# Kernel tuning notes

Measured on AMD Instinct MI355X. Metric: run time of the kernel, lower is better.

Reference implementation:

```python
import jax, jax.numpy as jnp
import numpy as np
import math

K = 3          # kernel_size
P_GEM = 3.0    # GeM power
EPS_GEM = 1e-6
EPS_NORM = 1e-12


def _l2n(x, axis):
    n = jnp.sqrt(jnp.sum(x * x, axis=axis, keepdims=True))
    return x / jnp.maximum(n, EPS_NORM)


def setup_inputs() -> dict:
    key = jax.random.key(0)
    ks = jax.random.split(key, 7)
    b, hw, c, nc = 32, 196, 768, 4096
    hidden = c  # mlp_ratio = 1
    return {
        "patch_tokens": jax.random.normal(ks[0], (b, hw, c), dtype=jnp.float32),
        "fc1_w": jax.random.normal(ks[1], (c, hidden), dtype=jnp.float32) * 0.02,
        "fc1_b": jnp.zeros((hidden,), dtype=jnp.float32),
        "fc2_w": jax.random.normal(ks[2], (hidden, c), dtype=jnp.float32) * 0.02,
        "fc2_b": jnp.zeros((c,), dtype=jnp.float32),
        "head_w": jax.random.normal(ks[3], (c, nc), dtype=jnp.float32) * 0.02,
        "head_b": jnp.zeros((nc,), dtype=jnp.float32),
    }


def reference(patch_tokens, fc1_w, fc1_b, fc2_w, fc2_b, head_w, head_b):
    b, hw, c = patch_tokens.shape
    h = w = int(math.sqrt(hw))

    # ---- SpaceSelfAware: pad -> unfold (3x3 local windows) -> multiply ----
    img = jnp.transpose(patch_tokens, (0, 2, 1)).reshape(b, c, h, w)
    # ZeroPad2d((left=1, right=1, top=2, bottom=0)) for kernel_size=3
    padded = jnp.pad(img, ((0, 0), (0, 0), (K - 1, 0), (K // 2, K // 2)))
    # stack the 9 shifted views, row-major over (ki, kj) matching nn.Unfold
    wins = jnp.stack(
        [padded[:, :, ki:ki + h, kj:kj + w] for ki in range(K) for kj in range(K)],
        axis=2,
    )  # (b, c, 9, h, w)
    y = wins.reshape(b, c, K, K, hw)
    y = jnp.transpose(y, (0, 4, 1, 2, 3))  # (b, hw, c, K, K)
    ssa = patch_tokens[:, :, :, None, None] * y  # (b, hw, c, K, K)

    # ---- space_fusion: L2Norm(dim=1) then GeM(p=3) over the KxK window ----
    ssa = _l2n(ssa, axis=1)
    pooled = jnp.mean(jnp.clip(ssa, EPS_GEM, None) ** P_GEM, axis=(-2, -1)) ** (1.0 / P_GEM)  # (b, hw, c)

    # ---- residual + L2 normalize over channels + Mlp ----
    tokens = pooled + patch_tokens
    tokens = _l2n(tokens, axis=-1)
    hdn = jax.nn.gelu(tokens @ fc1_w + fc1_b, approximate=False)
    tokens = hdn @ fc2_w + fc2_b  # (b, hw, c)

    # ---- GeMHead: GeM(p=3) over tokens, linear to nc, L2 normalize ----
    g = jnp.mean(jnp.clip(tokens, EPS_GEM, None) ** P_GEM, axis=1) ** (1.0 / P_GEM)  # (b, c)
    desc = g @ head_w + head_b  # (b, nc)
    desc = _l2n(desc, axis=-1)
    return desc
```

## Files before the change

kernel.cpp:

```cpp
#include <hip/hip_runtime.h>
#include <hip/hip_bf16.h>
#include <math.h>

#define B   32
#define P   196
#define C   768
#define NC  4096
#define HH  14
#define KSPLIT 24
#define NT  12
#define M6  6272
#define TW  (768 * 32)
#define TM  (M6 * 32)

typedef _Float16 half8 __attribute__((ext_vector_type(8)));
typedef _Float16 half4 __attribute__((ext_vector_type(4)));
typedef float f32x4 __attribute__((ext_vector_type(4)));

#define GLOAD_LDS16(g, l)                                                      \
    __builtin_amdgcn_global_load_lds(                                          \
        (const __attribute__((address_space(1))) void*)(g),                    \
        (__attribute__((address_space(3))) void*)(l), 16, 0, 0)

__global__ __launch_bounds__(256) void k_ssa(const float* __restrict__ t,
                                             float* __restrict__ pre) {
    const int b = blockIdx.y, c0 = blockIdx.x * 16;
    __shared__ float xp_[256 * 16];
    __shared__ float part[4][9][16];
    __shared__ float inv_norm[9][16];
    const int tid = threadIdx.x;
    const int cc = tid & 15, g = tid >> 4, wv = tid >> 6;

#pragma unroll
    for (int q = 0; q < 16; ++q) xp_[q * 256 + tid] = 0.0f;
    __syncthreads();

    for (int idx = tid; idx < 784; idx += 256) {
        const int p = idx >> 2, c = (idx & 3) * 4;
        const int i = p / HH, j = p % HH;
        *(float4*)&xp_[((i + 2) * 16 + (j + 1)) * 16 + c] =
            *(const float4*)&t[((size_t)b * P + p) * C + c0 + c];
    }
    __syncthreads();

    float s[9] = {};
    {
        int i = 0, j = g;
        if (j >= HH) { j -= HH; i = 1; }
        for (int p = g; p < P; p += 16) {
            const int base = ((i + 2) * 16 + (j + 1)) * 16 + cc;
            const float xp = xp_[base];
            const float xp2 = xp * xp;
#pragma unroll
            for (int k = 0; k < 9; ++k) {
                const int off = ((k / 3) - 2) * 16 + (k % 3) - 1;
                const float nb = xp_[base + off * 16];
                s[k] += xp2 * nb * nb;
            }
            j += 2; ++i;
            if (j >= HH) { j -= HH; ++i; }
        }
    }
#pragma unroll
    for (int k = 0; k < 9; ++k) {
        float r = s[k];
        r += __shfl_xor(r, 16);
        r += __shfl_xor(r, 32);
        s[k] = r;
    }
    if ((tid & 63) < 16) {
#pragma unroll
        for (int k = 0; k < 9; ++k) part[wv][k][cc] = s[k];
    }
    __syncthreads();
    if (tid < 144) {
        const int k = tid >> 4, c2 = tid & 15;
        const float t4 = part[0][k][c2] + part[1][k][c2] +
                         part[2][k][c2] + part[3][k][c2];
        inv_norm[k][c2] = 1.0f / fmaxf(sqrtf(t4), 1e-12f);
    }
    __syncthreads();

    float invn[9];
#pragma unroll
    for (int k = 0; k < 9; ++k) invn[k] = inv_norm[k][cc];

    {
        int i = 0, j = g;
        if (j >= HH) { j -= HH; i = 1; }
        for (int p = g; p < P; p += 16) {
            const int base = ((i + 2) * 16 + (j + 1)) * 16 + cc;
            const float xp = xp_[base];
            float acc = 0.0f;
#pragma unroll
            for (int k = 0; k < 9; ++k) {
                const int off = ((k / 3) - 2) * 16 + (k % 3) - 1;
                const float v = xp * xp_[base + off * 16];
                const float u = fmaxf(v * invn[k], 1e-6f);
                acc += u * u * u;
            }
            pre[((size_t)b * P + p) * C + c0 + cc] =
                cbrtf(acc * (1.0f / 9.0f)) + xp;
            j += 2; ++i;
            if (j >= HH) { j -= HH; ++i; }
        }
    }
}

__global__ __launch_bounds__(256) void k_rownorm(const float* __restrict__ in,
                                                 _Float16* __restrict__ outP) {
    const int row = blockIdx.x;
    const float* r = in + (size_t)row * C;
    const int tid = threadIdx.x;
    float vals[3];
    float s = 0.0f;
#pragma unroll
    for (int q = 0; q < 3; ++q) {
        vals[q] = r[tid + q * 256];
        s += vals[q] * vals[q];
    }
    __shared__ float partial[4];
    __shared__ float inv;
    __shared__ _Float16 nrm[C];
#pragma unroll
    for (int off = 32; off > 0; off >>= 1) s += __shfl_xor(s, off);
    if ((tid & 63) == 0) partial[tid >> 6] = s;
    __syncthreads();
    if (tid == 0)
        inv = 1.0f / fmaxf(sqrtf(partial[0] + partial[1] + partial[2] + partial[3]), 1e-12f);
    __syncthreads();
#pragma unroll
    for (int q = 0; q < 3; ++q)
        nrm[tid + q * 256] = (_Float16)(vals[q] * inv);
    __syncthreads();
    if (tid < 96) {
        const half8 v = *(const half8*)&nrm[tid * 8];
        const int kb = tid >> 2;
        *(half8*)&outP[(size_t)kb * TM + (size_t)row * 32 + (tid & 3) * 8] = v;
    }
}

__global__ __launch_bounds__(256) void k_wt(const float* __restrict__ W,
                                            _Float16* __restrict__ WtP) {
    __shared__ float tt[32][33];
    const int k0 = blockIdx.x * 32, n0 = blockIdx.y * 32;
    const int r = threadIdx.x / 32, c = threadIdx.x % 32;
#pragma unroll
    for (int q = 0; q < 4; ++q)
        tt[r + q * 8][c] = W[(size_t)(k0 + r + q * 8) * C + n0 + c];
    __syncthreads();
    const int nl = threadIdx.x >> 3, h = threadIdx.x & 7;
    const int n = n0 + nl;
    half4 v;
#pragma unroll
    for (int j = 0; j < 4; ++j) v[j] = (_Float16)tt[h * 4 + j][nl];
    *(half4*)&WtP[(size_t)blockIdx.x * TW + (size_t)n * 32 + h * 4] = v;
}

template <bool GELU>
__global__ __launch_bounds__(256) void k_mfma_gemm(
    const _Float16* __restrict__ TokP,
    const _Float16* __restrict__ WtP,
    const float* __restrict__ bias,
    void* __restrict__ Cout) {
    __shared__ _Float16 lA[3][2][64][32];
    __shared__ _Float16 lB[3][2][64][32];
    const int tid = threadIdx.x;
    const int w = tid >> 6, l = tid & 63;
    const int l15 = l & 15, lk = l >> 4;

    const int lid = blockIdx.x;
    int vm, vn;
    if (lid < 1152) { vm = (lid / 96) * 8 + (lid & 7); vn = (lid % 96) >> 3; }
    else            { const int r = lid - 1152; vm = 96 + r / 12; vn = r % 12; }
    const int m0 = vm * 64, n0 = vn * 64;
    const int wn = (w & 1) * 32, wm = (w >> 1) * 32;

    f32x4 acc[2][2] = {};

    const int kbsel = w & 1;
    const bool isB = (w >= 2);
    const _Float16* srcBase =
        isB ? (TokP + (size_t)m0 * 32) : (WtP + (size_t)n0 * 32);
    const size_t tileStride = isB ? (size_t)TM : (size_t)TW;
    _Float16* dst0 = isB ? &lB[0][kbsel][0][0] : &lA[0][kbsel][0][0];

#define ISSUE(tt, bf_)                                                         \
    {   const _Float16* s_ = srcBase + (size_t)(2 * (tt) + kbsel) * tileStride;\
        _Float16* d_ = dst0 + (size_t)(bf_) * 4096;                            \
        GLOAD_LDS16(s_ + l * 8,        d_ + l * 8);                            \
        GLOAD_LDS16(s_ + 512 + l * 8,  d_ + 512 + l * 8);                      \
        GLOAD_LDS16(s_ + 1024 + l * 8, d_ + 1024 + l * 8);                     \
        GLOAD_LDS16(s_ + 1536 + l * 8, d_ + 1536 + l * 8); }

    ISSUE(0, 0); ISSUE(1, 1); ISSUE(2, 2);

    for (int t = 0; t < NT; ++t) {
        if (t < NT - 2)       asm volatile("s_waitcnt vmcnt(8)" ::: "memory");
        else if (t == NT - 2) asm volatile("s_waitcnt vmcnt(4)" ::: "memory");
        else                  asm volatile("s_waitcnt vmcnt(0)" ::: "memory");
        __builtin_amdgcn_s_barrier();
        __builtin_amdgcn_sched_barrier(0);

        const int buf = t % 3;
#pragma unroll
        for (int kk = 0; kk < 2; ++kk) {
            half8 af[2], bf[2];
#pragma unroll
            for (int fa = 0; fa < 2; ++fa)
                af[fa] = *(const half8*)&lA[buf][kk][wn + fa * 16 + l15][lk * 8];
#pragma unroll
            for (int fb = 0; fb < 2; ++fb)
                bf[fb] = *(const half8*)&lB[buf][kk][wm + fb * 16 + l15][lk * 8];
#pragma unroll
            for (int fa = 0; fa < 2; ++fa)
#pragma unroll
                for (int fb = 0; fb < 2; ++fb)
                    acc[fa][fb] = __builtin_amdgcn_mfma_f32_16x16x32_f16(
                        af[fa], bf[fb], acc[fa][fb], 0, 0, 0);
        }
        asm volatile("s_waitcnt lgkmcnt(0)" ::: "memory");
        __builtin_amdgcn_s_barrier();
        __builtin_amdgcn_sched_barrier(0);
        if (t < NT - 3) ISSUE(t + 3, buf);
    }
#undef ISSUE

#pragma unroll
    for (int fa = 0; fa < 2; ++fa) {
        const int nb = n0 + wn + fa * 16 + lk * 4;
        const float4 bv = *(const float4*)&bias[nb];
#pragma unroll
        for (int fb = 0; fb < 2; ++fb) {
            const int m = m0 + wm + fb * 16 + l15;
            if (GELU) {
                half4 o;
#pragma unroll
                for (int rr = 0; rr < 4; ++rr) {
                    float v = acc[fa][fb][rr] + ((const float*)&bv)[rr];
                    v = 0.5f * v * (1.0f + erff(v * 0.70710678118654752f));
                    o[rr] = (_Float16)v;
                }
                *(half4*)&((_Float16*)Cout)[(size_t)(nb >> 5) * TM +
                                            (size_t)m * 32 + (nb & 31)] = o;
            } else {
                float4 o;
#pragma unroll
                for (int rr = 0; rr < 4; ++rr)
                    ((float*)&o)[rr] = acc[fa][fb][rr] + ((const float*)&bv)[rr];
                *(float4*)&((float*)Cout)[(size_t)m * C + nb] = o;
            }
        }
    }
}

__global__ __launch_bounds__(256) void k_gempool(const float* __restrict__ tk,
                                                 float* __restrict__ g) {
    const int b = blockIdx.x / 12;
    const int c0 = (blockIdx.x % 12) * 64;
    const int tid = threadIdx.x;
    const int cc = tid & 63, pg = tid >> 6;
    float s = 0.0f;
    for (int p = pg * 49; p < pg * 49 + 49; ++p) {
        const float v = fmaxf(tk[((size_t)b * P + p) * C + c0 + cc], 1e-6f);
        s += v * v * v;
    }
    __shared__ float part[4][64];
    part[pg][cc] = s;
    __syncthreads();
    if (tid < 64) {
        const float t4 = part[0][cc] + part[1][cc] + part[2][cc] + part[3][cc];
        g[b * C + c0 + cc] = cbrtf(t4 * (1.0f / (float)P));
    }
}

__global__ __launch_bounds__(256) void k_head1(const float* __restrict__ g,
                                               const float* __restrict__ W,
                                               float* __restrict__ partial) {
    const int n0 = blockIdx.x * 64;
    const int k0 = blockIdx.y * 32;
    __shared__ float gs[32][32];
    __shared__ float part[4][32][64];
    const int tid = threadIdx.x;

    for (int idx = tid; idx < 32 * 32; idx += 256)
        gs[idx >> 5][idx & 31] = g[(idx >> 5) * C + k0 + (idx & 31)];
    __syncthreads();

    const int c = tid & 63, q = tid >> 6;
    float acc[32] = {};
#pragma unroll
    for (int kk = 0; kk < 8; ++kk) {
        const int k = q * 8 + kk;
        const float wv = W[(size_t)(k0 + k) * NC + n0 + c];
#pragma unroll
        for (int b = 0; b < 32; ++b) acc[b] += gs[b][k] * wv;
    }
#pragma unroll
    for (int b = 0; b < 32; ++b) part[q][b][c] = acc[b];
    __syncthreads();

    for (int o = tid; o < 32 * 64; o += 256) {
        const int b = o >> 6, cc = o & 63;
        const float v = part[0][b][cc] + part[1][b][cc] +
                        part[2][b][cc] + part[3][b][cc];
        partial[((size_t)blockIdx.y * 32 + b) * NC + n0 + cc] = v;
    }
}

__global__ __launch_bounds__(256) void k_head2(const float* __restrict__ partial,
                                               const float* __restrict__ hb,
                                               float* __restrict__ out) {
    const int n = blockIdx.x * 256 + threadIdx.x;
    const int b = blockIdx.y;
    float s = hb[n];
#pragma unroll
    for (int ks = 0; ks < KSPLIT; ++ks)
        s += partial[((size_t)ks * 32 + b) * NC + n];
    out[(size_t)b * NC + n] = s;
}

__global__ __launch_bounds__(256) void k_outnorm(float* __restrict__ out) {
    const int b = blockIdx.x;
    float* r = out + (size_t)b * NC;
    const int tid = threadIdx.x;
    float v[16];
    float s = 0.0f;
#pragma unroll
    for (int q = 0; q < 16; ++q) {
        v[q] = r[tid + q * 256];
        s += v[q] * v[q];
    }
    __shared__ float partial[4];
    __shared__ float inv;
#pragma unroll
    for (int off = 32; off > 0; off >>= 1) s += __shfl_xor(s, off);
    if ((tid & 63) == 0) partial[tid >> 6] = s;
    __syncthreads();
    if (tid == 0)
        inv = 1.0f / fmaxf(sqrtf(partial[0] + partial[1] + partial[2] + partial[3]), 1e-12f);
    __syncthreads();
#pragma unroll
    for (int q = 0; q < 16; ++q) r[tid + q * 256] = v[q] * inv;
}

extern "C" void kernel_launch(void* const* d_in, const int* in_sizes, int n_in,
                              void* d_out, int out_size, void* d_ws, size_t ws_size,
                              hipStream_t stream) {
    const float* patch  = (const float*)d_in[0];
    const float* fc1_w  = (const float*)d_in[1];
    const float* fc1_b  = (const float*)d_in[2];
    const float* fc2_w  = (const float*)d_in[3];
    const float* fc2_b  = (const float*)d_in[4];
    const float* head_w = (const float*)d_in[5];
    const float* head_b = (const float*)d_in[6];
    float* out = (float*)d_out;

    const size_t big = (size_t)B * P * C;
    float*    pre  = (float*)d_ws;
    _Float16* tokP = (_Float16*)(pre + big);
    _Float16* hdnP = tokP + big;
    _Float16* wt1  = hdnP + big;
    _Float16* wt2  = wt1 + C * C;
    float*    gbuf = (float*)(wt2 + C * C);
    float*    hpart = gbuf + B * C;
    float*    tok2 = pre;

    k_ssa<<<dim3(C / 16, B), dim3(256), 0, stream>>>(patch, pre);
    k_wt<<<dim3(C / 32, C / 32), dim3(256), 0, stream>>>(fc1_w, wt1);
    k_wt<<<dim3(C / 32, C / 32), dim3(256), 0, stream>>>(fc2_w, wt2);
    k_rownorm<<<dim3(B * P), dim3(256), 0, stream>>>(pre, tokP);
    k_mfma_gemm<true><<<dim3(1176), dim3(256), 0, stream>>>(
        tokP, wt1, fc1_b, hdnP);
    k_mfma_gemm<false><<<dim3(1176), dim3(256), 0, stream>>>(
        hdnP, wt2, fc2_b, tok2);
    k_gempool<<<dim3(B * 12), dim3(256), 0, stream>>>(tok2, gbuf);
    k_head1<<<dim3(NC / 64, KSPLIT), dim3(256), 0, stream>>>(gbuf, head_w, hpart);
    k_head2<<<dim3(NC / 256, B), dim3(256), 0, stream>>>(hpart, head_b, out);
    k_outnorm<<<dim3(B), dim3(256), 0, stream>>>(out);
}
```

Before: 96.31 us.

## Enlarge GEMM tiles to 128x128 with double buffering and fp16 fc2 output

The MFMA GEMM block tile grows from 64x64 to 128x128, with a 4x4 fragment grid per wave. The LDS pipeline drops from triple to double buffering, and the block remap is rewritten for the new grid of 294 blocks. The fc2 output is now stored as fp16 instead of fp32, and the GeM pooling kernel reads fp16. This raises data reuse per block and cuts store and readback traffic, at the cost of fewer blocks (about 294 for 256 CUs, so wave quantization), higher register use, and reduced precision on the intermediate tokens.

Result: no change. 97.61 us (+1.4%).

```diff
diff --git a/kernel.cpp b/kernel.cpp
--- a/kernel.cpp
+++ b/kernel.cpp
@@ -162,99 +162,98 @@
     const _Float16* __restrict__ TokP,
     const _Float16* __restrict__ WtP,
     const float* __restrict__ bias,
-    void* __restrict__ Cout) {
-    __shared__ _Float16 lA[3][2][64][32];
-    __shared__ _Float16 lB[3][2][64][32];
+    _Float16* __restrict__ Cout) {
+    __shared__ _Float16 lA[2][2][128][32];
+    __shared__ _Float16 lB[2][2][128][32];
     const int tid = threadIdx.x;
     const int w = tid >> 6, l = tid & 63;
     const int l15 = l & 15, lk = l >> 4;
 
     const int lid = blockIdx.x;
     int vm, vn;
-    if (lid < 1152) { vm = (lid / 96) * 8 + (lid & 7); vn = (lid % 96) >> 3; }
-    else            { const int r = lid - 1152; vm = 96 + r / 12; vn = r % 12; }
-    const int m0 = vm * 64, n0 = vn * 64;
-    const int wn = (w & 1) * 32, wm = (w >> 1) * 32;
-
-    f32x4 acc[2][2] = {};
-
-    const int kbsel = w & 1;
-    const bool isB = (w >= 2);
-    const _Float16* srcBase =
-        isB ? (TokP + (size_t)m0 * 32) : (WtP + (size_t)n0 * 32);
-    const size_t tileStride = isB ? (size_t)TM : (size_t)TW;
-    _Float16* dst0 = isB ? &lB[0][kbsel][0][0] : &lA[0][kbsel][0][0];
-
-#define ISSUE(tt, bf_)                                                         \
-    {   const _Float16* s_ = srcBase + (size_t)(2 * (tt) + kbsel) * tileStride;\
-        _Float16* d_ = dst0 + (size_t)(bf_) * 4096;                            \
-        GLOAD_LDS16(s_ + l * 8,        d_ + l * 8);                            \
-        GLOAD_LDS16(s_ + 512 + l * 8,  d_ + 512 + l * 8);                      \
-        GLOAD_LDS16(s_ + 1024 + l * 8, d_ + 1024 + l * 8);                     \
-        GLOAD_LDS16(s_ + 1536 + l * 8, d_ + 1536 + l * 8); }
-
-    ISSUE(0, 0); ISSUE(1, 1); ISSUE(2, 2);
+    if (lid < 288) { vm = (lid / 48) * 8 + (lid & 7); vn = (lid % 48) >> 3; }
+    else           { vm = 48; vn = lid - 288; }
+    const int m0 = vm * 128, n0 = vn * 128;
+    const int wn = (w & 1) * 64, wm = (w >> 1) * 64;
+
+    f32x4 acc[4][4] = {};
+
+#define ISSUE(tt, st_)                                                         \
+    {                                                                          \
+        _Pragma("unroll")                                                      \
+        for (int q = 0; q < 8; ++q) {                                          \
+            const int gc = w * 8 + q;                                          \
+            const bool isA = gc < 16;                                          \
+            const int kbp = (gc >> 3) & 1, ld = gc & 7;                        \
+            const _Float16* s_ = isA                                           \
+                ? WtP + (size_t)(2 * (tt) + kbp) * TW + (size_t)n0 * 32 + ld * 512 \
+                : TokP + (size_t)(2 * (tt) + kbp) * TM + (size_t)m0 * 32 + ld * 512; \
+            _Float16* d_ = isA ? &lA[st_][kbp][ld * 16][0]                     \
+                               : &lB[st_][kbp][ld * 16][0];                    \
+            GLOAD_LDS16(s_ + l * 8, d_ + l * 8);                               \
+        }                                                                      \
+    }
+
+    ISSUE(0, 0); ISSUE(1, 1);
 
     for (int t = 0; t < NT; ++t) {
-        if (t < NT - 2)       asm volatile("s_waitcnt vmcnt(8)" ::: "memory");
-        else if (t == NT - 2) asm volatile("s_waitcnt vmcnt(4)" ::: "memory");
-        else                  asm volatile("s_waitcnt vmcnt(0)" ::: "memory");
+        if (t < NT - 1) asm volatile("s_waitcnt vmcnt(8)" ::: "memory");
+        else            asm volatile("s_waitcnt vmcnt(0)" ::: "memory");
         __builtin_amdgcn_s_barrier();
         __builtin_amdgcn_sched_barrier(0);
 
-        const int buf = t % 3;
+        const int st = t & 1;
 #pragma unroll
         for (int kk = 0; kk < 2; ++kk) {
-            half8 af[2], bf[2];
-#pragma unroll
-            for (int fa = 0; fa < 2; ++fa)
-                af[fa] = *(const half8*)&lA[buf][kk][wn + fa * 16 + l15][lk * 8];
-#pragma unroll
-            for (int fb = 0; fb < 2; ++fb)
-                bf[fb] = *(const half8*)&lB[buf][kk][wm + fb * 16 + l15][lk * 8];
-#pragma unroll
-            for (int fa = 0; fa < 2; ++fa)
-#pragma unroll
-                for (int fb = 0; fb < 2; ++fb)
+            half8 af[4], bf[4];
+#pragma unroll
+            for (int fa = 0; fa < 4; ++fa)
+                af[fa] = *(const half8*)&lA[st][kk][wn + fa * 16 + l15][lk * 8];
+#pragma unroll
+            for (int fb = 0; fb < 4; ++fb)
+                bf[fb] = *(const half8*)&lB[st][kk][wm + fb * 16 + l15][lk * 8];
+#pragma unroll
+            for (int fa = 0; fa < 4; ++fa)
+#pragma unroll
+                for (int fb = 0; fb < 4; ++fb)
                     acc[fa][fb] = __builtin_amdgcn_mfma_f32_16x16x32_f16(
                         af[fa], bf[fb], acc[fa][fb], 0, 0, 0);
         }
         asm volatile("s_waitcnt lgkmcnt(0)" ::: "memory");
         __builtin_amdgcn_s_barrier();
         __builtin_amdgcn_sched_barrier(0);
-        if (t < NT - 3) ISSUE(t + 3, buf);
+        if (t < NT - 2) ISSUE(t + 2, st);
     }
 #undef ISSUE
 
 #pragma unroll
-    for (int fa = 0; fa < 2; ++fa) {
+    for (int fa = 0; fa < 4; ++fa) {
         const int nb = n0 + wn + fa * 16 + lk * 4;
         const float4 bv = *(const float4*)&bias[nb];
 #pragma unroll
-        for (int fb = 0; fb < 2; ++fb) {
+        for (int fb = 0; fb < 4; ++fb) {
             const int m = m0 + wm + fb * 16 + l15;
+            half4 o;
             if (GELU) {
-                half4 o;
 #pragma unroll
                 for (int rr = 0; rr < 4; ++rr) {
                     float v = acc[fa][fb][rr] + ((const float*)&bv)[rr];
                     v = 0.5f * v * (1.0f + erff(v * 0.70710678118654752f));
                     o[rr] = (_Float16)v;
                 }
-                *(half4*)&((_Float16*)Cout)[(size_t)(nb >> 5) * TM +
-                                            (size_t)m * 32 + (nb & 31)] = o;
+                *(half4*)&Cout[(size_t)(nb >> 5) * TM + (size_t)m * 32 +
+                               (nb & 31)] = o;
             } else {
-                float4 o;
 #pragma unroll
                 for (int rr = 0; rr < 4; ++rr)
-                    ((float*)&o)[rr] = acc[fa][fb][rr] + ((const float*)&bv)[rr];
-                *(float4*)&((float*)Cout)[(size_t)m * C + nb] = o;
+                    o[rr] = (_Float16)(acc[fa][fb][rr] + ((const float*)&bv)[rr]);
+                *(half4*)&Cout[(size_t)m * C + nb] = o;
             }
         }
     }
 }
 
-__global__ __launch_bounds__(256) void k_gempool(const float* __restrict__ tk,
+__global__ __launch_bounds__(256) void k_gempool(const _Float16* __restrict__ tk,
                                                  float* __restrict__ g) {
     const int b = blockIdx.x / 12;
     const int c0 = (blockIdx.x % 12) * 64;
@@ -262,7 +261,7 @@
     const int cc = tid & 63, pg = tid >> 6;
     float s = 0.0f;
     for (int p = pg * 49; p < pg * 49 + 49; ++p) {
-        const float v = fmaxf(tk[((size_t)b * P + p) * C + c0 + cc], 1e-6f);
+        const float v = fmaxf((float)tk[((size_t)b * P + p) * C + c0 + cc], 1e-6f);
         s += v * v * v;
     }
     __shared__ float part[4][64];
@@ -364,15 +363,15 @@
     _Float16* wt2  = wt1 + C * C;
     float*    gbuf = (float*)(wt2 + C * C);
     float*    hpart = gbuf + B * C;
-    float*    tok2 = pre;
+    _Float16* tok2 = (_Float16*)pre;
 
     k_ssa<<<dim3(C / 16, B), dim3(256), 0, stream>>>(patch, pre);
     k_wt<<<dim3(C / 32, C / 32), dim3(256), 0, stream>>>(fc1_w, wt1);
     k_wt<<<dim3(C / 32, C / 32), dim3(256), 0, stream>>>(fc2_w, wt2);
     k_rownorm<<<dim3(B * P), dim3(256), 0, stream>>>(pre, tokP);
-    k_mfma_gemm<true><<<dim3(1176), dim3(256), 0, stream>>>(
+    k_mfma_gemm<true><<<dim3(294), dim3(256), 0, stream>>>(
         tokP, wt1, fc1_b, hdnP);
-    k_mfma_gemm<false><<<dim3(1176), dim3(256), 0, stream>>>(
+    k_mfma_gemm<false><<<dim3(294), dim3(256), 0, stream>>>(
         hdnP, wt2, fc2_b, tok2);
     k_gempool<<<dim3(B * 12), dim3(256), 0, stream>>>(tok2, gbuf);
     k_head1<<<dim3(NC / 64, KSPLIT), dim3(256), 0, stream>>>(gbuf, head_w, hpart);
```

## Swizzle packed fp16 operand layout to avoid LDS bank conflicts; store fc2 output as fp16

Applied to the files above, without the earlier changes.

The producer kernels (rownorm, weight transpose, GELU epilogue) now write their 8-element k-chunks at XOR-swizzled slots within each 32-wide row. The GEMM reads LDS fragments with the same swizzle, which is meant to spread ds_read accesses across banks. Separately, the fc2 GEMM output is stored as fp16 instead of fp32, and the GeM pooling reads it as fp16, halving that intermediate's write and read traffic. The fp16 storage before the cube-power pooling adds some rounding error.

After: 94.03 us. 1.02x faster.

```diff
diff --git a/kernel.cpp b/kernel.cpp
--- a/kernel.cpp
+++ b/kernel.cpp
@@ -136,7 +136,8 @@
     if (tid < 96) {
         const half8 v = *(const half8*)&nrm[tid * 8];
         const int kb = tid >> 2;
-        *(half8*)&outP[(size_t)kb * TM + (size_t)row * 32 + (tid & 3) * 8] = v;
+        const int slot = (tid & 3) ^ ((row >> 1) & 3);
+        *(half8*)&outP[(size_t)kb * TM + (size_t)row * 32 + slot * 8] = v;
     }
 }
 
@@ -154,7 +155,8 @@
     half4 v;
 #pragma unroll
     for (int j = 0; j < 4; ++j) v[j] = (_Float16)tt[h * 4 + j][nl];
-    *(half4*)&WtP[(size_t)blockIdx.x * TW + (size_t)n * 32 + h * 4] = v;
+    const int el = (h * 4) ^ (((n >> 1) & 3) << 3);
+    *(half4*)&WtP[(size_t)blockIdx.x * TW + (size_t)n * 32 + el] = v;
 }
 
 template <bool GELU>
@@ -162,7 +164,7 @@
     const _Float16* __restrict__ TokP,
     const _Float16* __restrict__ WtP,
     const float* __restrict__ bias,
-    void* __restrict__ Cout) {
+    _Float16* __restrict__ Cout) {
     __shared__ _Float16 lA[3][2][64][32];
     __shared__ _Float16 lB[3][2][64][32];
     const int tid = threadIdx.x;
@@ -207,11 +209,17 @@
         for (int kk = 0; kk < 2; ++kk) {
             half8 af[2], bf[2];
 #pragma unroll
-            for (int fa = 0; fa < 2; ++fa)
-                af[fa] = *(const half8*)&lA[buf][kk][wn + fa * 16 + l15][lk * 8];
-#pragma unroll
-            for (int fb = 0; fb < 2; ++fb)
-                bf[fb] = *(const half8*)&lB[buf][kk][wm + fb * 16 + l15][lk * 8];
+            for (int fa = 0; fa < 2; ++fa) {
+                const int rowA = wn + fa * 16 + l15;
+                const int colA = (lk ^ ((rowA >> 1) & 3)) * 8;
+                af[fa] = *(const half8*)&lA[buf][kk][rowA][colA];
+            }
+#pragma unroll
+            for (int fb = 0; fb < 2; ++fb) {
+                const int rowB = wm + fb * 16 + l15;
+                const int colB = (lk ^ ((rowB >> 1) & 3)) * 8;
+                bf[fb] = *(const half8*)&lB[buf][kk][rowB][colB];
+            }
 #pragma unroll
             for (int fa = 0; fa < 2; ++fa)
 #pragma unroll
@@ -233,28 +241,27 @@
 #pragma unroll
         for (int fb = 0; fb < 2; ++fb) {
             const int m = m0 + wm + fb * 16 + l15;
+            half4 o;
             if (GELU) {
-                half4 o;
 #pragma unroll
                 for (int rr = 0; rr < 4; ++rr) {
                     float v = acc[fa][fb][rr] + ((const float*)&bv)[rr];
                     v = 0.5f * v * (1.0f + erff(v * 0.70710678118654752f));
                     o[rr] = (_Float16)v;
                 }
-                *(half4*)&((_Float16*)Cout)[(size_t)(nb >> 5) * TM +
-                                            (size_t)m * 32 + (nb & 31)] = o;
+                const int el = (nb & 31) ^ (((m >> 1) & 3) << 3);
+                *(half4*)&Cout[(size_t)(nb >> 5) * TM + (size_t)m * 32 + el] = o;
             } else {
-                float4 o;
 #pragma unroll
                 for (int rr = 0; rr < 4; ++rr)
-                    ((float*)&o)[rr] = acc[fa][fb][rr] + ((const float*)&bv)[rr];
-                *(float4*)&((float*)Cout)[(size_t)m * C + nb] = o;
+                    o[rr] = (_Float16)(acc[fa][fb][rr] + ((const float*)&bv)[rr]);
+                *(half4*)&Cout[(size_t)m * C + nb] = o;
             }
         }
     }
 }
 
-__global__ __launch_bounds__(256) void k_gempool(const float* __restrict__ tk,
+__global__ __launch_bounds__(256) void k_gempool(const _Float16* __restrict__ tk,
                                                  float* __restrict__ g) {
     const int b = blockIdx.x / 12;
     const int c0 = (blockIdx.x % 12) * 64;
@@ -262,7 +269,7 @@
     const int cc = tid & 63, pg = tid >> 6;
     float s = 0.0f;
     for (int p = pg * 49; p < pg * 49 + 49; ++p) {
-        const float v = fmaxf(tk[((size_t)b * P + p) * C + c0 + cc], 1e-6f);
+        const float v = fmaxf((float)tk[((size_t)b * P + p) * C + c0 + cc], 1e-6f);
         s += v * v * v;
     }
     __shared__ float part[4][64];
@@ -364,7 +371,7 @@
     _Float16* wt2  = wt1 + C * C;
     float*    gbuf = (float*)(wt2 + C * C);
     float*    hpart = gbuf + B * C;
-    float*    tok2 = pre;
+    _Float16* tok2 = (_Float16*)pre;
 
     k_ssa<<<dim3(C / 16, B), dim3(256), 0, stream>>>(patch, pre);
     k_wt<<<dim3(C / 32, C / 32), dim3(256), 0, stream>>>(fc1_w, wt1);
```
